# Kernel tuning notes

Hardware: AMD Instinct MI355X
Metric: run time of the kernel (lower is better)

Reference implementation:

```python
import jax, jax.numpy as jnp
import numpy as np

B, L, D, Z, V, N, C = 4, 4096, 1024, 128, 1024, 16, 128
STD = 0.02
LN_EPS = 1e-5


def setup_inputs() -> dict:
    ks = jax.random.split(jax.random.key(0), 12)
    f32 = jnp.float32
    return {
        "x": jax.random.normal(ks[0], (B, L, D), dtype=f32),
        "ln1_g": jnp.ones((D,), f32), "ln1_b": jnp.zeros((D,), f32),
        "delta": jax.random.normal(ks[1], (D, N, 1), dtype=f32),
        "alpha": jax.random.normal(ks[2], (D, N, 1), dtype=f32),
        "beta_e": jax.random.normal(ks[3], (D, N, 1), dtype=f32) * STD,
        "gamma_e": jax.random.normal(ks[4], (D, N), dtype=f32),
        "omega": jax.random.normal(ks[5], (D,), dtype=f32) * STD,
        "Wv": jax.random.normal(ks[6], (D, V), dtype=f32) * STD, "bv": jnp.zeros((V,), f32),
        "Wmx": jax.random.normal(ks[7], (D, Z + V + 2 * D), dtype=f32) * STD, "bmx": jnp.zeros((Z + V + 2 * D,), f32),
        "Wh": jax.random.normal(ks[8], (V, D), dtype=f32) * STD, "bh": jnp.zeros((D,), f32),
        "gamma_g": jax.random.normal(ks[9], (2, Z), dtype=f32) * STD, "beta_g": jnp.zeros((2, Z), f32),
        "rpb": jax.random.normal(ks[10], (2 * C - 1,), dtype=f32) * STD,
        "ln2_g": jnp.ones((D,), f32), "ln2_b": jnp.zeros((D,), f32),
        "W1": jax.random.normal(ks[11], (D, 2 * D), dtype=f32) * STD, "b1": jnp.zeros((2 * D,), f32),
        "W2": jax.random.normal(jax.random.fold_in(ks[11], 1), (2 * D, D), dtype=f32) * STD, "b2": jnp.zeros((D,), f32),
    }


def layer_norm(x, g, b):
    m = jnp.mean(x, axis=-1, keepdims=True)
    xc = x - m
    v = jnp.mean(xc * xc, axis=-1, keepdims=True)
    return xc * jax.lax.rsqrt(v + LN_EPS) * g + b


def multi_head_ema(x, delta, alpha, beta_e, gamma_e, omega):
    # x: (B,L,D). Damped EMA SSM (MEGA), unidirectional, via causal FFT conv.
    p = jax.nn.sigmoid(delta)                      # (D,N,1)
    a = jax.nn.sigmoid(alpha)                      # (D,N,1)
    q = 1.0 - p * a                                # decay in (0,1)
    t = jnp.arange(L, dtype=x.dtype)               # (L,)
    vander = t[None, None, :] * jnp.log(q)         # (D,N,L)
    kern = (p * beta_e) * jnp.exp(vander)          # (D,N,L)
    scale = (1.0 / N) ** 0.5
    k = jnp.einsum('dnl,dn->dl', kern, gamma_e * scale)  # (D,L)
    n_fft = 2 * L
    xf = jnp.fft.rfft(x.transpose(0, 2, 1), n=n_fft)     # (B,D,F)
    kf = jnp.fft.rfft(k, n=n_fft)                        # (D,F)
    out = jnp.fft.irfft(xf * kf[None], n=n_fft)[..., :L] # (B,D,L) causal conv
    return out.transpose(0, 2, 1) + x * omega[None, None, :]


def simple_rel_pos_bias(rpb, c):
    # rpb: (2c-1,) -> (c,c) Toeplitz relative-position bias (MEGA 'simple')
    t = jnp.pad(rpb, (0, c))           # (3c-1,)
    t = jnp.tile(t, c)[:-c]            # (c*(3c-2),)
    t = t.reshape(c, 3 * c - 2)
    r = (2 * c - 1) // 2
    return t[:, r: t.shape[1] - r]     # (c,c)


def reference(x, ln1_g, ln1_b, delta, alpha, beta_e, gamma_e, omega, Wv, bv,
              Wmx, bmx, Wh, bh, gamma_g, beta_g, rpb, ln2_g, ln2_b, W1, b1, W2, b2):
    residual = x
    xn = layer_norm(x, ln1_g, ln1_b)                         # prenorm
    v = jax.nn.silu(xn @ Wv + bv)                            # (B,L,V)
    mx = jax.nn.silu(multi_head_ema(xn, delta, alpha, beta_e, gamma_e, omega))
    base = mx @ Wmx + bmx                                    # (B,L,D+Z+V+D)
    u = jax.nn.sigmoid(base[..., :D])                        # gate
    zr = jax.nn.silu(base[..., D:D + Z + V])
    hx = base[..., D + Z + V:]                               # (B,L,D)
    z, r = zr[..., :Z], zr[..., Z:]                          # (B,L,Z),(B,L,V)
    zz = z[..., None, :] * gamma_g + beta_g                  # (B,L,2,Z)
    q, k = zz[..., 0, :], zz[..., 1, :]
    K = L // C
    qc = q.reshape(B, K, C, Z) * (Z ** -0.5)
    kc = k.reshape(B, K, C, Z)
    vc = v.reshape(B, K, C, V)
    bias = simple_rel_pos_bias(rpb, C)                       # (C,C)
    scores = jnp.einsum('bkcz,bkdz->bkcd', qc, kc) + bias    # (B,K,C,C)
    attn = jax.nn.softmax(scores, axis=-1)
    h = jnp.einsum('bkcd,bkdv->bkcv', attn, vc).reshape(B, L, V)
    h = jax.nn.silu(hx + (h * r) @ Wh + bh)                  # (B,L,D)
    out = residual + u * (h - residual)                      # addcmul gate
    # FFN residual block (prenorm, residual 'R')
    y = layer_norm(out, ln2_g, ln2_b)
    y = jax.nn.silu(y @ W1 + b1) @ W2 + b2
    return out + y
```

## Files before the change

kernel.cpp:

```cpp
#include <hip/hip_runtime.h>
#include <hip/hip_bf16.h>

typedef __attribute__((ext_vector_type(8))) short bf16x8;
typedef __attribute__((ext_vector_type(4))) float f32x4;

#define DEV static __device__ __forceinline__

#define VMW(n) asm volatile("s_waitcnt vmcnt(" #n ")" ::: "memory")
#define BARX   asm volatile("s_barrier" ::: "memory")

DEV float bf2f(unsigned short u) {
    unsigned int x = ((unsigned int)u) << 16;
    return __builtin_bit_cast(float, x);
}
DEV unsigned short f2bf(float f) {
    unsigned int x = __builtin_bit_cast(unsigned int, f);
    unsigned int r = x + 0x7fffu + ((x >> 16) & 1u);
    return (unsigned short)(r >> 16);
}
DEV float sigmoidf_(float x) { return 1.f / (1.f + __expf(-x)); }
DEV float siluf_(float x)    { return x / (1.f + __expf(-x)); }

DEV void llds16(const unsigned short* g, unsigned short* l) {
    __builtin_amdgcn_global_load_lds((const __attribute__((address_space(1))) void*)g,
                                     (__attribute__((address_space(3))) void*)l, 16, 0, 0);
}

DEV void swz_xy(int& bx, int& by) {
    int gx = gridDim.x;
    int ychunk = gridDim.y >> 3;
    int n = blockIdx.y * gx + blockIdx.x;
    int idx = n >> 3;
    bx = idx / ychunk;
    by = (n & 7) * ychunk + (idx % ychunk);
}

DEV void mfma256(const unsigned short* __restrict__ A, const unsigned short* __restrict__ Bt,
                 int lda, int ldb, int KT, unsigned short* lds, f32x4 (&acc)[8][4])
{
    const int tid  = threadIdx.x;
    const int lane = tid & 63;
    const int w    = tid >> 6;
    const int wr   = (w >> 2) << 6;
    const int wc   = (w & 3) << 5;
    const int mr   = lane & 15;
    const int kq   = (lane >> 4) << 4;
    const int srow = tid >> 3;
    const int sw   = ((tid & 7) ^ (srow & 7)) << 3;

    const unsigned short* gA0 = A + (size_t)srow * lda + sw;
    const unsigned short* gA1 = gA0 + (size_t)128 * lda;
    const unsigned short* gB0 = Bt + (size_t)srow * ldb + sw;
    const unsigned short* gB1 = gB0 + (size_t)128 * ldb;
    const size_t a64 = (size_t)64 * lda, b64 = (size_t)64 * ldb;
    unsigned short* dst = lds + tid * 8;

    const int swz = (mr & 7) << 4;
    const int offK0 = kq ^ swz;
    const int offK1 = (64 + kq) ^ swz;
    const char* pAb = (const char*)lds + (wr + mr) * 128;
    const char* pBb = (const char*)lds + 32768 + (wc + mr) * 128;

#define STAGE8(NX) do { \
    unsigned short* d0 = dst + (NX) * 32768; \
    llds16(gA0, d0);          llds16(gA0 + a64, d0 + 4096);  gA0 += 64; \
    llds16(gB0, d0 + 16384);  llds16(gB0 + b64, d0 + 20480); gB0 += 64; \
    llds16(gB1, d0 + 24576);  llds16(gB1 + b64, d0 + 28672); gB1 += 64; \
    llds16(gA1, d0 + 8192);   llds16(gA1 + a64, d0 + 12288); gA1 += 64; \
} while (0)

    STAGE8(0);

    bf16x8 av[4][2], bA[2][2], bB[2][2];
    for (int kt = 0; kt < KT; ++kt) {
        VMW(0);
        BARX;
        if (kt + 1 < KT) STAGE8((kt & 1) ^ 1);
        const char* pA_ = pAb + (kt & 1) * 65536;
        const char* pB_ = pBb + (kt & 1) * 65536;
#pragma unroll
        for (int m = 0; m < 4; ++m) { av[m][0] = *(const bf16x8*)(pA_ + m * 2048 + offK0);
                                      av[m][1] = *(const bf16x8*)(pA_ + m * 2048 + offK1); }
#pragma unroll
        for (int n = 0; n < 2; ++n) { bA[n][0] = *(const bf16x8*)(pB_ + n * 2048 + offK0);
                                      bA[n][1] = *(const bf16x8*)(pB_ + n * 2048 + offK1); }
        __builtin_amdgcn_s_setprio(1);
#pragma unroll
        for (int m = 0; m < 4; ++m)
#pragma unroll
            for (int n = 0; n < 2; ++n) {
                acc[m][n] = __builtin_amdgcn_mfma_f32_16x16x32_bf16(av[m][0], bA[n][0], acc[m][n], 0, 0, 0);
                acc[m][n] = __builtin_amdgcn_mfma_f32_16x16x32_bf16(av[m][1], bA[n][1], acc[m][n], 0, 0, 0);
            }
        __builtin_amdgcn_s_setprio(0);
#pragma unroll
        for (int n = 0; n < 2; ++n) { bB[n][0] = *(const bf16x8*)(pB_ + 16384 + n * 2048 + offK0);
                                      bB[n][1] = *(const bf16x8*)(pB_ + 16384 + n * 2048 + offK1); }
        __builtin_amdgcn_s_setprio(1);
#pragma unroll
        for (int m = 0; m < 4; ++m)
#pragma unroll
            for (int n = 0; n < 2; ++n) {
                acc[m][2 + n] = __builtin_amdgcn_mfma_f32_16x16x32_bf16(av[m][0], bB[n][0], acc[m][2 + n], 0, 0, 0);
                acc[m][2 + n] = __builtin_amdgcn_mfma_f32_16x16x32_bf16(av[m][1], bB[n][1], acc[m][2 + n], 0, 0, 0);
            }
        __builtin_amdgcn_s_setprio(0);
#pragma unroll
        for (int m = 0; m < 4; ++m) { av[m][0] = *(const bf16x8*)(pA_ + 16384 + m * 2048 + offK0);
                                      av[m][1] = *(const bf16x8*)(pA_ + 16384 + m * 2048 + offK1); }
        __builtin_amdgcn_s_setprio(1);
#pragma unroll
        for (int m = 0; m < 4; ++m)
#pragma unroll
            for (int n = 0; n < 2; ++n) {
                acc[4 + m][n] = __builtin_amdgcn_mfma_f32_16x16x32_bf16(av[m][0], bA[n][0], acc[4 + m][n], 0, 0, 0);
                acc[4 + m][n] = __builtin_amdgcn_mfma_f32_16x16x32_bf16(av[m][1], bA[n][1], acc[4 + m][n], 0, 0, 0);
            }
        __builtin_amdgcn_s_setprio(0);
        __builtin_amdgcn_s_setprio(1);
#pragma unroll
        for (int m = 0; m < 4; ++m)
#pragma unroll
            for (int n = 0; n < 2; ++n) {
                acc[4 + m][2 + n] = __builtin_amdgcn_mfma_f32_16x16x32_bf16(av[m][0], bB[n][0], acc[4 + m][2 + n], 0, 0, 0);
                acc[4 + m][2 + n] = __builtin_amdgcn_mfma_f32_16x16x32_bf16(av[m][1], bB[n][1], acc[4 + m][2 + n], 0, 0, 0);
            }
        __builtin_amdgcn_s_setprio(0);
    }
#undef STAGE8
    BARX;
}

template <class F>
DEV void stage_rm(unsigned short* lds, const f32x4 (&acc)[8][4], F f)
{
    const int lane = threadIdx.x & 63, w = threadIdx.x >> 6;
    const int wr = (w >> 2) << 6, wc = (w & 3) << 5;
    const int rsub = (lane >> 4) << 2, csub = lane & 15;
#pragma unroll
    for (int i = 0; i < 8; ++i)
#pragma unroll
        for (int j = 0; j < 4; ++j) {
            int rl = ((i >> 2) << 7) + wr + ((i & 3) << 4) + rsub;
            int cl = ((j >> 1) << 7) + wc + ((j & 1) << 4) + csub;
#pragma unroll
            for (int jj = 0; jj < 4; ++jj) {
                int r = rl + jj;
                *(unsigned short*)((char*)lds + r * 512 + ((cl * 2) ^ (((r >> 2) & 3) << 5))) =
                    f(acc[i][j][jj], cl);
            }
        }
}
template <class F>
DEV void stage_cm(unsigned short* lds, const f32x4 (&acc)[8][4], F f)
{
    const int lane = threadIdx.x & 63, w = threadIdx.x >> 6;
    const int wr = (w >> 2) << 6, wc = (w & 3) << 5;
    const int rsub = (lane >> 4) << 2, csub = lane & 15;
#pragma unroll
    for (int i = 0; i < 8; ++i)
#pragma unroll
        for (int j = 0; j < 4; ++j) {
            int rl = ((i >> 2) << 7) + wr + ((i & 3) << 4) + rsub;
            int cl = ((j >> 1) << 7) + wc + ((j & 1) << 4) + csub;
            ushort4 p;
            p.x = f(acc[i][j][0], cl); p.y = f(acc[i][j][1], cl);
            p.z = f(acc[i][j][2], cl); p.w = f(acc[i][j][3], cl);
            *(ushort4*)((char*)lds + cl * 512 + ((rl * 2) ^ ((cl & 3) << 4))) = p;
        }
}
DEV bf16x8 rd_rm(const unsigned short* lds, int row, int cb) {
    return *(const bf16x8*)((const char*)lds + row * 512 + ((cb * 16) ^ (((row >> 2) & 3) << 5)));
}
DEV bf16x8 rd_cm(const unsigned short* lds, int col, int rb) {
    return *(const bf16x8*)((const char*)lds + col * 512 + ((rb * 16) ^ ((col & 3) << 4)));
}

DEV void mfma_loop(const unsigned short* __restrict__ A, const unsigned short* __restrict__ Bt,
                   int lda, int ldb, int K, unsigned short* lds, f32x4 acc[4][4])
{
    const int tid = threadIdx.x;
    const int lane = tid & 63;
    const int wid = tid >> 6;
    const int wm = wid >> 1, wn = wid & 1;
    const int row0 = tid >> 2,         cg0 = (tid & 3) * 8;
    const int row1 = (256 + tid) >> 2, cg1 = (tid & 3) * 8;
    const int dst0 = (tid - lane) * 8;
    const int dst1 = (256 + tid - lane) * 8;

    auto stage = [&](unsigned short* sbuf, int kt) {
        const unsigned short* gA = A + (size_t)kt * 32;
        const unsigned short* gB = Bt + (size_t)kt * 32;
        llds16(gA + (size_t)row0 * lda + cg0, sbuf + dst0);
        llds16(gA + (size_t)row1 * lda + cg1, sbuf + dst1);
        llds16(gB + (size_t)row0 * ldb + cg0, sbuf + 4096 + dst0);
        llds16(gB + (size_t)row1 * ldb + cg1, sbuf + 4096 + dst1);
    };

    const int KT = K >> 5;
    stage(lds, 0);
    __syncthreads();
    const int mr = lane & 15, kr = (lane >> 4) * 8;
    for (int kt = 0; kt < KT; ++kt) {
        unsigned short* sbuf = lds + (kt & 1) * 8192;
        if (kt + 1 < KT) stage(lds + ((kt + 1) & 1) * 8192, kt + 1);
        const unsigned short* sA = sbuf;
        const unsigned short* sB = sbuf + 4096;
        bf16x8 av[4], bv[4];
#pragma unroll
        for (int f = 0; f < 4; ++f) {
            av[f] = *(const bf16x8*)(sA + (wm * 64 + f * 16 + mr) * 32 + kr);
            bv[f] = *(const bf16x8*)(sB + (wn * 64 + f * 16 + mr) * 32 + kr);
        }
#pragma unroll
        for (int fm = 0; fm < 4; ++fm)
#pragma unroll
            for (int fn = 0; fn < 4; ++fn)
                acc[fm][fn] = __builtin_amdgcn_mfma_f32_16x16x32_bf16(av[fm], bv[fn], acc[fm][fn], 0, 0, 0);
        __syncthreads();
    }
}

__global__ void k_transpose(const float* __restrict__ W, unsigned short* __restrict__ Wt, int K, int N)
{
    __shared__ float tile[32][33];
    int n0 = blockIdx.x * 32, k0 = blockIdx.y * 32;
    for (int i = threadIdx.y; i < 32; i += 8)
        tile[i][threadIdx.x] = W[(size_t)(k0 + i) * N + n0 + threadIdx.x];
    __syncthreads();
    for (int i = threadIdx.y; i < 32; i += 8)
        Wt[(size_t)(n0 + i) * K + k0 + threadIdx.x] = f2bf(tile[threadIdx.x][i]);
}

__global__ __launch_bounds__(256) void k_ln(const float* __restrict__ x, const float* __restrict__ g,
                                            const float* __restrict__ b, unsigned short* __restrict__ o)
{
    size_t row = blockIdx.x;
    int tid = threadIdx.x;
    float4 v = ((const float4*)(x + row * 1024))[tid];
    float s = v.x + v.y + v.z + v.w;
    float sq = v.x * v.x + v.y * v.y + v.z * v.z + v.w * v.w;
#pragma unroll
    for (int off = 1; off < 64; off <<= 1) { s += __shfl_xor(s, off); sq += __shfl_xor(sq, off); }
    __shared__ float ls[4], lq[4];
    int wid = tid >> 6;
    if ((tid & 63) == 0) { ls[wid] = s; lq[wid] = sq; }
    __syncthreads();
    s = ls[0] + ls[1] + ls[2] + ls[3];
    sq = lq[0] + lq[1] + lq[2] + lq[3];
    float mean = s * (1.f / 1024.f);
    float var = sq * (1.f / 1024.f) - mean * mean;
    float rstd = rsqrtf(var + 1e-5f);
    float4 gv = ((const float4*)g)[tid];
    float4 bv = ((const float4*)b)[tid];
    ushort4 p;
    p.x = f2bf((v.x - mean) * rstd * gv.x + bv.x);
    p.y = f2bf((v.y - mean) * rstd * gv.y + bv.y);
    p.z = f2bf((v.z - mean) * rstd * gv.z + bv.z);
    p.w = f2bf((v.w - mean) * rstd * gv.w + bv.w);
    ((ushort4*)(o + row * 1024))[tid] = p;
}

#define SEG 128
#define NSEG 32

__global__ __launch_bounds__(64) void k_ema_a(const unsigned short* __restrict__ xn,
                                              const float* __restrict__ delta, const float* __restrict__ alpha,
                                              float* __restrict__ st)
{
    int d = blockIdx.x * 64 + threadIdx.x;
    int s = blockIdx.y, b = blockIdx.z;
    float q[16], h[16];
#pragma unroll
    for (int n = 0; n < 16; ++n) {
        float p = sigmoidf_(delta[d * 16 + n]);
        float a = sigmoidf_(alpha[d * 16 + n]);
        q[n] = 1.f - p * a; h[n] = 0.f;
    }
    const unsigned short* xp = xn + ((size_t)b * 4096 + (size_t)s * SEG) * 1024 + d;
    for (int l = 0; l < SEG; ++l) {
        float xv = bf2f(xp[(size_t)l * 1024]);
#pragma unroll
        for (int n = 0; n < 16; ++n) h[n] = q[n] * h[n] + xv;
    }
    float* sp = st + (size_t)(b * 1024 + d) * 16 * NSEG;
#pragma unroll
    for (int n = 0; n < 16; ++n) sp[n * NSEG + s] = h[n];
}

__global__ void k_ema_b(const float* __restrict__ delta, const float* __restrict__ alpha, float* __restrict__ st)
{
    int gid = blockIdx.x * 256 + threadIdx.x;
    int n = gid & 15, d = (gid >> 4) & 1023;
    float p = sigmoidf_(delta[d * 16 + n]);
    float a = sigmoidf_(alpha[d * 16 + n]);
    float qq = 1.f - p * a;
    float qs = qq;
#pragma unroll
    for (int i = 0; i < 7; ++i) qs *= qs;
    float* sp = st + (size_t)gid * NSEG;
    float A_ = 0.f;
#pragma unroll
    for (int s = 0; s < NSEG; ++s) { float t = sp[s]; sp[s] = A_; A_ = qs * A_ + t; }
}

__global__ __launch_bounds__(64) void k_ema_c(const unsigned short* __restrict__ xn,
                                              const float* __restrict__ delta, const float* __restrict__ alpha,
                                              const float* __restrict__ beta_e, const float* __restrict__ gamma_e,
                                              const float* __restrict__ omega, const float* __restrict__ st,
                                              unsigned short* __restrict__ mxb)
{
    int d = blockIdx.x * 64 + threadIdx.x;
    int s = blockIdx.y, b = blockIdx.z;
    float q[16], c[16], h[16];
    const float* sp = st + (size_t)(b * 1024 + d) * 16 * NSEG;
#pragma unroll
    for (int n = 0; n < 16; ++n) {
        float p = sigmoidf_(delta[d * 16 + n]);
        float a = sigmoidf_(alpha[d * 16 + n]);
        q[n] = 1.f - p * a;
        c[n] = p * beta_e[d * 16 + n] * gamma_e[d * 16 + n] * 0.25f;
        h[n] = sp[n * NSEG + s];
    }
    float om = omega[d];
    const unsigned short* xp = xn + ((size_t)b * 4096 + (size_t)s * SEG) * 1024 + d;
    unsigned short* op = mxb + ((size_t)b * 4096 + (size_t)s * SEG) * 1024 + d;
    for (int l = 0; l < SEG; ++l) {
        float xv = bf2f(xp[(size_t)l * 1024]);
        float o = xv * om;
#pragma unroll
        for (int n = 0; n < 16; ++n) { h[n] = q[n] * h[n] + xv; o += c[n] * h[n]; }
        op[(size_t)l * 1024] = f2bf(siluf_(o));
    }
}

__global__ __launch_bounds__(512, 2) void k_gemm_v2_v(const unsigned short* __restrict__ xn,
                                                      const unsigned short* __restrict__ WvT,
                                                      const float* __restrict__ bv, unsigned short* __restrict__ vt)
{
    __shared__ __align__(16) unsigned short lds[65536];
    int bx, by; swz_xy(bx, by);
    int n0 = bx * 256, m0 = by * 256;
    f32x4 acc[8][4] = {};
    mfma256(xn + (size_t)m0 * 1024, WvT + (size_t)n0 * 1024, 1024, 1024, 16, lds, acc);
    stage_cm(lds, acc, [&](float v, int cl) -> unsigned short {
        return f2bf(siluf_(v + bv[n0 + cl]));
    });
    __syncthreads();
    const int t = threadIdx.x;
#pragma unroll
    for (int it = 0; it < 16; ++it) {
        int col = it * 16 + (t >> 5);
        int rb = t & 31;
        bf16x8 vv = rd_cm(lds, col, rb);
        int grow = m0 + rb * 8;
        size_t off = ((size_t)(grow >> 7) * 1024 + (n0 + col)) * 128 + (grow & 127);
        *(bf16x8*)(vt + off) = vv;
    }
}

__global__ __launch_bounds__(512, 2) void k_gemm_v2_mx(const unsigned short* __restrict__ mx,
                                                       const unsigned short* __restrict__ WmxT,
                                                       const float* __restrict__ bmx,
                                                       const float* __restrict__ gamma_g, const float* __restrict__ beta_g,
                                                       unsigned short* __restrict__ ub, unsigned short* __restrict__ qb,
                                                       unsigned short* __restrict__ kb, unsigned short* __restrict__ rb,
                                                       unsigned short* __restrict__ hxb)
{
    __shared__ __align__(16) unsigned short lds[65536];
    int bx, by; swz_xy(bx, by);
    int n0 = bx * 256, m0 = by * 256;
    f32x4 acc[8][4] = {};
    mfma256(mx + (size_t)m0 * 1024, WmxT + (size_t)n0 * 1024, 1024, 1024, 16, lds, acc);
    stage_rm(lds, acc, [&](float v, int cl) -> unsigned short {
        int gc = n0 + cl;
        if (gc >= 3200) return 0;
        float val = v + bmx[gc];
        if (gc < 1024) return f2bf(sigmoidf_(val));
        if (gc < 2176) return f2bf(siluf_(val));
        return f2bf(val);
    });
    __syncthreads();
    const int t = threadIdx.x;
#pragma unroll
    for (int it = 0; it < 16; ++it) {
        int row = it * 16 + (t >> 5);
        int cb = t & 31;
        int gc = n0 + cb * 8;
        if (gc >= 3200) continue;
        bf16x8 vv = rd_rm(lds, row, cb);
        size_t grow = m0 + row;
        if (gc < 1024) {
            *(bf16x8*)(ub + grow * 1024 + gc) = vv;
        } else if (gc < 1152) {
            int zc = gc - 1024;
            bf16x8 qv, kv;
#pragma unroll
            for (int e = 0; e < 8; ++e) {
                float z = bf2f((unsigned short)vv[e]);
                qv[e] = (short)f2bf((z * gamma_g[zc + e] + beta_g[zc + e]) * 0.088388347648318447f);
                kv[e] = (short)f2bf(z * gamma_g[128 + zc + e] + beta_g[128 + zc + e]);
            }
            *(bf16x8*)(qb + grow * 128 + zc) = qv;
            *(bf16x8*)(kb + grow * 128 + zc) = kv;
        } else if (gc < 2176) {
            *(bf16x8*)(rb + grow * 1024 + (gc - 1152)) = vv;
        } else {
            *(bf16x8*)(hxb + grow * 1024 + (gc - 2176)) = vv;
        }
    }
}

__global__ __launch_bounds__(256) void k_attn(const unsigned short* __restrict__ qb,
                                              const unsigned short* __restrict__ kb,
                                              const float* __restrict__ rpb, unsigned short* __restrict__ attn)
{
    __shared__ __align__(16) union U { unsigned short stage[16384]; unsigned short sc[128 * 132]; } sh;
    int bc = blockIdx.x;
    size_t t0 = (size_t)bc * 128;
    f32x4 acc[4][4] = {};
    mfma_loop(qb + t0 * 128, kb + t0 * 128, 128, 128, 128, sh.stage, acc);
    int tid = threadIdx.x, lane = tid & 63, wid = tid >> 6, wm = wid >> 1, wn = wid & 1;
#pragma unroll
    for (int fm = 0; fm < 4; ++fm)
#pragma unroll
        for (int fn = 0; fn < 4; ++fn) {
            int r = wm * 64 + fm * 16 + ((lane >> 4) << 2);
            int c = wn * 64 + fn * 16 + (lane & 15);
#pragma unroll
            for (int j = 0; j < 4; ++j) sh.sc[(r + j) * 132 + c] = f2bf(acc[fm][fn][j]);
        }
    __syncthreads();
    int row = tid >> 1, half = tid & 1;
    const unsigned short* srow = sh.sc + row * 132 + half * 64;
    const float* bp = rpb + 127 - row + half * 64;
    float v[64];
    float mxv = -1e30f;
#pragma unroll
    for (int i = 0; i < 64; ++i) { float s = bf2f(srow[i]) + bp[i]; v[i] = s; mxv = fmaxf(mxv, s); }
    mxv = fmaxf(mxv, __shfl_xor(mxv, 1));
    float sum = 0.f;
#pragma unroll
    for (int i = 0; i < 64; ++i) { float e = __expf(v[i] - mxv); v[i] = e; sum += e; }
    sum += __shfl_xor(sum, 1);
    float inv = 1.f / sum;
    unsigned short* arow = attn + ((size_t)bc * 128 + row) * 128 + half * 64;
#pragma unroll
    for (int i = 0; i < 64; ++i) arow[i] = f2bf(v[i] * inv);
}

__global__ __launch_bounds__(256) void k_gemm_pv(const unsigned short* __restrict__ attn,
                                                 const unsigned short* __restrict__ vt,
                                                 unsigned short* __restrict__ rhr)
{
    __shared__ __align__(16) unsigned short lds[16384];
    int bc = blockIdx.z;
    int n0 = blockIdx.x * 128;
    f32x4 acc[4][4] = {};
    mfma_loop(attn + (size_t)bc * 16384, vt + (size_t)bc * 131072 + (size_t)n0 * 128, 128, 128, 128, lds, acc);
    int lane = threadIdx.x & 63, wid = threadIdx.x >> 6, wm = wid >> 1, wn = wid & 1;
#pragma unroll
    for (int fm = 0; fm < 4; ++fm)
#pragma unroll
        for (int fn = 0; fn < 4; ++fn) {
            int rowb = wm * 64 + fm * 16 + ((lane >> 4) << 2);
            int col = n0 + wn * 64 + fn * 16 + (lane & 15);
#pragma unroll
            for (int j = 0; j < 4; ++j) {
                size_t m = (size_t)bc * 128 + rowb + j;
                size_t off = m * 1024 + col;
                rhr[off] = f2bf(acc[fm][fn][j] * bf2f(rhr[off]));
            }
        }
}

__global__ __launch_bounds__(512, 2) void k_gemm_v2_out(const unsigned short* __restrict__ hr,
                                                        const unsigned short* __restrict__ WhT,
                                                        const float* __restrict__ bh,
                                                        const unsigned short* __restrict__ hxb,
                                                        const unsigned short* __restrict__ ub,
                                                        const float* __restrict__ x, float* __restrict__ outp)
{
    __shared__ __align__(16) unsigned short lds[65536];
    int bx, by; swz_xy(bx, by);
    int n0 = bx * 256, m0 = by * 256;
    f32x4 acc[8][4] = {};
    mfma256(hr + (size_t)m0 * 1024, WhT + (size_t)n0 * 1024, 1024, 1024, 16, lds, acc);
    const int lane = threadIdx.x & 63, w = threadIdx.x >> 6;
    const int wr = (w >> 2) << 6, wc = (w & 3) << 5;
    const int rsub = (lane >> 4) << 2, csub = lane & 15;
#pragma unroll
    for (int i = 0; i < 8; ++i)
#pragma unroll
        for (int j = 0; j < 4; ++j) {
            int rowb = m0 + ((i >> 2) << 7) + wr + ((i & 3) << 4) + rsub;
            int col = n0 + ((j >> 1) << 7) + wc + ((j & 1) << 4) + csub;
            float bias = bh[col];
#pragma unroll
            for (int jj = 0; jj < 4; ++jj) {
                size_t off = (size_t)(rowb + jj) * 1024 + col;
                float g = acc[i][j][jj] + bias + bf2f(hxb[off]);
                float h2 = siluf_(g);
                float xv = x[off];
                outp[off] = xv + bf2f(ub[off]) * (h2 - xv);
            }
        }
}

__global__ __launch_bounds__(512, 2) void k_ffn1_v2(const unsigned short* __restrict__ yn,
                                                    const unsigned short* __restrict__ W1T,
                                                    const float* __restrict__ b1, unsigned short* __restrict__ t1)
{
    __shared__ __align__(16) unsigned short lds[65536];
    int bx, by; swz_xy(bx, by);
    int n0 = bx * 256, m0 = by * 256;
    f32x4 acc[8][4] = {};
    mfma256(yn + (size_t)m0 * 1024, W1T + (size_t)n0 * 1024, 1024, 1024, 16, lds, acc);
    stage_rm(lds, acc, [&](float v, int cl) -> unsigned short {
        return f2bf(siluf_(v + b1[n0 + cl]));
    });
    __syncthreads();
    const int t = threadIdx.x;
#pragma unroll
    for (int it = 0; it < 16; ++it) {
        int row = it * 16 + (t >> 5);
        int cb = t & 31;
        bf16x8 vv = rd_rm(lds, row, cb);
        *(bf16x8*)(t1 + (size_t)(m0 + row) * 2048 + n0 + cb * 8) = vv;
    }
}

__global__ __launch_bounds__(512, 2) void k_ffn2_v2(const unsigned short* __restrict__ t1,
                                                    const unsigned short* __restrict__ W2T,
                                                    const float* __restrict__ b2, float* __restrict__ outp)
{
    __shared__ __align__(16) unsigned short lds[65536];
    int bx, by; swz_xy(bx, by);
    int n0 = bx * 256, m0 = by * 256;
    f32x4 acc[8][4] = {};
    mfma256(t1 + (size_t)m0 * 2048, W2T + (size_t)n0 * 2048, 2048, 2048, 32, lds, acc);
    const int lane = threadIdx.x & 63, w = threadIdx.x >> 6;
    const int wr = (w >> 2) << 6, wc = (w & 3) << 5;
    const int rsub = (lane >> 4) << 2, csub = lane & 15;
#pragma unroll
    for (int i = 0; i < 8; ++i)
#pragma unroll
        for (int j = 0; j < 4; ++j) {
            int rowb = m0 + ((i >> 2) << 7) + wr + ((i & 3) << 4) + rsub;
            int col = n0 + ((j >> 1) << 7) + wc + ((j & 1) << 4) + csub;
            float bias = b2[col];
#pragma unroll
            for (int jj = 0; jj < 4; ++jj) {
                size_t off = (size_t)(rowb + jj) * 1024 + col;
                outp[off] = outp[off] + acc[i][j][jj] + bias;
            }
        }
}

extern "C" void kernel_launch(void* const* d_in, const int* in_sizes, int n_in,
                              void* d_out, int out_size, void* d_ws, size_t ws_size,
                              hipStream_t stream)
{
    (void)in_sizes; (void)n_in; (void)out_size; (void)ws_size;
    const float* x      = (const float*)d_in[0];
    const float* ln1_g  = (const float*)d_in[1];
    const float* ln1_b  = (const float*)d_in[2];
    const float* delta  = (const float*)d_in[3];
    const float* alpha  = (const float*)d_in[4];
    const float* beta_e = (const float*)d_in[5];
    const float* gamma_e= (const float*)d_in[6];
    const float* omega  = (const float*)d_in[7];
    const float* Wv     = (const float*)d_in[8];
    const float* bv     = (const float*)d_in[9];
    const float* Wmx    = (const float*)d_in[10];
    const float* bmx    = (const float*)d_in[11];
    const float* Wh     = (const float*)d_in[12];
    const float* bh     = (const float*)d_in[13];
    const float* gamma_g= (const float*)d_in[14];
    const float* beta_g = (const float*)d_in[15];
    const float* rpb    = (const float*)d_in[16];
    const float* ln2_g  = (const float*)d_in[17];
    const float* ln2_b  = (const float*)d_in[18];
    const float* W1     = (const float*)d_in[19];
    const float* b1     = (const float*)d_in[20];
    const float* W2     = (const float*)d_in[21];
    const float* b2     = (const float*)d_in[22];
    float* outp = (float*)d_out;

    char* w = (char*)d_ws;
    unsigned short* xn   = (unsigned short*)(w + 0);
    unsigned short* at   = (unsigned short*)(w + 0);
    unsigned short* mxb  = (unsigned short*)(w + 33554432);
    unsigned short* t1   = (unsigned short*)(w + 0);
    unsigned short* vt   = (unsigned short*)(w + 67108864);
    unsigned short* ub   = (unsigned short*)(w + 100663296);
    unsigned short* hxb  = (unsigned short*)(w + 134217728);
    unsigned short* rb   = (unsigned short*)(w + 167772160);
    unsigned short* yn   = (unsigned short*)(w + 167772160);
    unsigned short* qb   = (unsigned short*)(w + 201326592);
    unsigned short* kb   = (unsigned short*)(w + 205520896);
    float*          st   = (float*)(w + 201326592);
    unsigned short* WvT  = (unsigned short*)(w + 209715200);
    unsigned short* WmxT = (unsigned short*)(w + 211812352);
    unsigned short* WhT  = (unsigned short*)(w + 218628096);
    unsigned short* W1T  = (unsigned short*)(w + 220725248);
    unsigned short* W2T  = (unsigned short*)(w + 224919552);

    dim3 tb(32, 8);
    k_transpose<<<dim3(32, 32), tb, 0, stream>>>(Wv, WvT, 1024, 1024);
    k_transpose<<<dim3(100, 32), tb, 0, stream>>>(Wmx, WmxT, 1024, 3200);
    k_transpose<<<dim3(32, 32), tb, 0, stream>>>(Wh, WhT, 1024, 1024);
    k_transpose<<<dim3(64, 32), tb, 0, stream>>>(W1, W1T, 1024, 2048);
    k_transpose<<<dim3(32, 64), tb, 0, stream>>>(W2, W2T, 2048, 1024);

    k_ln<<<16384, 256, 0, stream>>>(x, ln1_g, ln1_b, xn);

    k_ema_a<<<dim3(16, NSEG, 4), 64, 0, stream>>>(xn, delta, alpha, st);
    k_ema_b<<<256, 256, 0, stream>>>(delta, alpha, st);
    k_ema_c<<<dim3(16, NSEG, 4), 64, 0, stream>>>(xn, delta, alpha, beta_e, gamma_e, omega, st, mxb);

    k_gemm_v2_v<<<dim3(4, 64), 512, 0, stream>>>(xn, WvT, bv, vt);
    k_gemm_v2_mx<<<dim3(13, 64), 512, 0, stream>>>(mxb, WmxT, bmx, gamma_g, beta_g, ub, qb, kb, rb, hxb);
    k_attn<<<128, 256, 0, stream>>>(qb, kb, rpb, at);
    k_gemm_pv<<<dim3(8, 1, 128), 256, 0, stream>>>(at, vt, rb);
    k_gemm_v2_out<<<dim3(4, 64), 512, 0, stream>>>(rb, WhT, bh, hxb, ub, x, outp);
    k_ln<<<16384, 256, 0, stream>>>(outp, ln2_g, ln2_b, yn);
    k_ffn1_v2<<<dim3(8, 64), 512, 0, stream>>>(yn, W1T, b1, t1);
    k_ffn2_v2<<<dim3(4, 64), 512, 0, stream>>>(t1, W2T, b2, outp);
}
```

Before: 646.7 us.

## Use 16-wave 256x256 GEMM blocks with per-wave 64x64 tiles

Replaces the 8-wave 256x256 MFMA mainloop with a 16-wave (1024-thread) version where each wave owns a 64x64 sub-tile, halving accumulator registers per wave. It staggers the K-half order across waves to spread LDS bank traffic, uses __syncthreads instead of manual waitcnt/barrier, and splits the LDS-staged epilogues into two 128-row or 128-column halves because of the new wave layout. The aim is more waves in flight per CU for latency hiding. The trade-off is one block per CU instead of two, and full-block barriers each K step across 16 waves.

After: 1.162 ms. 79.7% more time.

```diff
diff --git a/kernel.cpp b/kernel.cpp
--- a/kernel.cpp
+++ b/kernel.cpp
@@ -5,9 +5,6 @@
 typedef __attribute__((ext_vector_type(4))) float f32x4;
 
 #define DEV static __device__ __forceinline__
-
-#define VMW(n) asm volatile("s_waitcnt vmcnt(" #n ")" ::: "memory")
-#define BARX   asm volatile("s_barrier" ::: "memory")
 
 DEV float bf2f(unsigned short u) {
     unsigned int x = ((unsigned int)u) << 16;
@@ -35,145 +32,72 @@
     by = (n & 7) * ychunk + (idx % ychunk);
 }
 
-DEV void mfma256(const unsigned short* __restrict__ A, const unsigned short* __restrict__ Bt,
-                 int lda, int ldb, int KT, unsigned short* lds, f32x4 (&acc)[8][4])
+DEV void mfma16w(const unsigned short* __restrict__ A, const unsigned short* __restrict__ Bt,
+                 int lda, int ldb, int KT, unsigned short* lds, f32x4 (&acc)[4][4])
 {
     const int tid  = threadIdx.x;
     const int lane = tid & 63;
     const int w    = tid >> 6;
-    const int wr   = (w >> 2) << 6;
-    const int wc   = (w & 3) << 5;
+    const int wm   = w >> 2, wn = w & 3;
     const int mr   = lane & 15;
-    const int kq   = (lane >> 4) << 4;
+    const int kg   = lane >> 4;
+
     const int srow = tid >> 3;
-    const int sw   = ((tid & 7) ^ (srow & 7)) << 3;
-
-    const unsigned short* gA0 = A + (size_t)srow * lda + sw;
+    const int sg   = (tid & 7) ^ (srow & 7);
+    const unsigned short* gA0 = A  + (size_t)srow * lda + sg * 8;
     const unsigned short* gA1 = gA0 + (size_t)128 * lda;
-    const unsigned short* gB0 = Bt + (size_t)srow * ldb + sw;
+    const unsigned short* gB0 = Bt + (size_t)srow * ldb + sg * 8;
     const unsigned short* gB1 = gB0 + (size_t)128 * ldb;
-    const size_t a64 = (size_t)64 * lda, b64 = (size_t)64 * ldb;
-    unsigned short* dst = lds + tid * 8;
-
-    const int swz = (mr & 7) << 4;
-    const int offK0 = kq ^ swz;
-    const int offK1 = (64 + kq) ^ swz;
-    const char* pAb = (const char*)lds + (wr + mr) * 128;
-    const char* pBb = (const char*)lds + 32768 + (wc + mr) * 128;
-
-#define STAGE8(NX) do { \
-    unsigned short* d0 = dst + (NX) * 32768; \
-    llds16(gA0, d0);          llds16(gA0 + a64, d0 + 4096);  gA0 += 64; \
-    llds16(gB0, d0 + 16384);  llds16(gB0 + b64, d0 + 20480); gB0 += 64; \
-    llds16(gB1, d0 + 24576);  llds16(gB1 + b64, d0 + 28672); gB1 += 64; \
-    llds16(gA1, d0 + 8192);   llds16(gA1 + a64, d0 + 12288); gA1 += 64; \
-} while (0)
-
-    STAGE8(0);
-
-    bf16x8 av[4][2], bA[2][2], bB[2][2];
+    unsigned short* dA0 = lds + tid * 8;
+    unsigned short* dA1 = dA0 + 8192;
+    unsigned short* dB0 = dA0 + 16384;
+    unsigned short* dB1 = dA0 + 24576;
+
+    const int swz  = (mr & 7) << 4;
+    const int off0 = (kg << 4) ^ swz;
+    const int off1 = (64 + (kg << 4)) ^ swz;
+    const char* pAr = (const char*)lds + (wm * 64 + mr) * 128;
+    const char* pBr = (const char*)lds + 32768 + (wn * 64 + mr) * 128;
+    const int stag = (w ^ (w >> 2)) & 1;
+
+    auto stage = [&](int nb) {
+        int o = nb * 32768;
+        llds16(gA0, dA0 + o); gA0 += 64;
+        llds16(gA1, dA1 + o); gA1 += 64;
+        llds16(gB0, dB0 + o); gB0 += 64;
+        llds16(gB1, dB1 + o); gB1 += 64;
+    };
+
+    bf16x8 av[4], bv[4];
+    auto halfK = [&](const char* pa, const char* pb, int off) {
+#pragma unroll
+        for (int f = 0; f < 4; ++f) {
+            av[f] = *(const bf16x8*)(pa + f * 2048 + off);
+            bv[f] = *(const bf16x8*)(pb + f * 2048 + off);
+        }
+        __builtin_amdgcn_s_setprio(1);
+#pragma unroll
+        for (int fm = 0; fm < 4; ++fm)
+#pragma unroll
+            for (int fn = 0; fn < 4; ++fn)
+                acc[fm][fn] = __builtin_amdgcn_mfma_f32_16x16x32_bf16(av[fm], bv[fn], acc[fm][fn], 0, 0, 0);
+        __builtin_amdgcn_s_setprio(0);
+    };
+
+    stage(0);
+    __syncthreads();
     for (int kt = 0; kt < KT; ++kt) {
-        VMW(0);
-        BARX;
-        if (kt + 1 < KT) STAGE8((kt & 1) ^ 1);
-        const char* pA_ = pAb + (kt & 1) * 65536;
-        const char* pB_ = pBb + (kt & 1) * 65536;
-#pragma unroll
-        for (int m = 0; m < 4; ++m) { av[m][0] = *(const bf16x8*)(pA_ + m * 2048 + offK0);
-                                      av[m][1] = *(const bf16x8*)(pA_ + m * 2048 + offK1); }
-#pragma unroll
-        for (int n = 0; n < 2; ++n) { bA[n][0] = *(const bf16x8*)(pB_ + n * 2048 + offK0);
-                                      bA[n][1] = *(const bf16x8*)(pB_ + n * 2048 + offK1); }
-        __builtin_amdgcn_s_setprio(1);
-#pragma unroll
-        for (int m = 0; m < 4; ++m)
-#pragma unroll
-            for (int n = 0; n < 2; ++n) {
-                acc[m][n] = __builtin_amdgcn_mfma_f32_16x16x32_bf16(av[m][0], bA[n][0], acc[m][n], 0, 0, 0);
-                acc[m][n] = __builtin_amdgcn_mfma_f32_16x16x32_bf16(av[m][1], bA[n][1], acc[m][n], 0, 0, 0);
-            }
-        __builtin_amdgcn_s_setprio(0);
-#pragma unroll
-        for (int n = 0; n < 2; ++n) { bB[n][0] = *(const bf16x8*)(pB_ + 16384 + n * 2048 + offK0);
-                                      bB[n][1] = *(const bf16x8*)(pB_ + 16384 + n * 2048 + offK1); }
-        __builtin_amdgcn_s_setprio(1);
-#pragma unroll
-        for (int m = 0; m < 4; ++m)
-#pragma unroll
-            for (int n = 0; n < 2; ++n) {
-                acc[m][2 + n] = __builtin_amdgcn_mfma_f32_16x16x32_bf16(av[m][0], bB[n][0], acc[m][2 + n], 0, 0, 0);
-                acc[m][2 + n] = __builtin_amdgcn_mfma_f32_16x16x32_bf16(av[m][1], bB[n][1], acc[m][2 + n], 0, 0, 0);
-            }
-        __builtin_amdgcn_s_setprio(0);
-#pragma unroll
-        for (int m = 0; m < 4; ++m) { av[m][0] = *(const bf16x8*)(pA_ + 16384 + m * 2048 + offK0);
-                                      av[m][1] = *(const bf16x8*)(pA_ + 16384 + m * 2048 + offK1); }
-        __builtin_amdgcn_s_setprio(1);
-#pragma unroll
-        for (int m = 0; m < 4; ++m)
-#pragma unroll
-            for (int n = 0; n < 2; ++n) {
-                acc[4 + m][n] = __builtin_amdgcn_mfma_f32_16x16x32_bf16(av[m][0], bA[n][0], acc[4 + m][n], 0, 0, 0);
-                acc[4 + m][n] = __builtin_amdgcn_mfma_f32_16x16x32_bf16(av[m][1], bA[n][1], acc[4 + m][n], 0, 0, 0);
-            }
-        __builtin_amdgcn_s_setprio(0);
-        __builtin_amdgcn_s_setprio(1);
-#pragma unroll
-        for (int m = 0; m < 4; ++m)
-#pragma unroll
-            for (int n = 0; n < 2; ++n) {
-                acc[4 + m][2 + n] = __builtin_amdgcn_mfma_f32_16x16x32_bf16(av[m][0], bB[n][0], acc[4 + m][2 + n], 0, 0, 0);
-                acc[4 + m][2 + n] = __builtin_amdgcn_mfma_f32_16x16x32_bf16(av[m][1], bB[n][1], acc[4 + m][2 + n], 0, 0, 0);
-            }
-        __builtin_amdgcn_s_setprio(0);
-    }
-#undef STAGE8
-    BARX;
-}
-
-template <class F>
-DEV void stage_rm(unsigned short* lds, const f32x4 (&acc)[8][4], F f)
-{
-    const int lane = threadIdx.x & 63, w = threadIdx.x >> 6;
-    const int wr = (w >> 2) << 6, wc = (w & 3) << 5;
-    const int rsub = (lane >> 4) << 2, csub = lane & 15;
-#pragma unroll
-    for (int i = 0; i < 8; ++i)
-#pragma unroll
-        for (int j = 0; j < 4; ++j) {
-            int rl = ((i >> 2) << 7) + wr + ((i & 3) << 4) + rsub;
-            int cl = ((j >> 1) << 7) + wc + ((j & 1) << 4) + csub;
-#pragma unroll
-            for (int jj = 0; jj < 4; ++jj) {
-                int r = rl + jj;
-                *(unsigned short*)((char*)lds + r * 512 + ((cl * 2) ^ (((r >> 2) & 3) << 5))) =
-                    f(acc[i][j][jj], cl);
-            }
-        }
-}
-template <class F>
-DEV void stage_cm(unsigned short* lds, const f32x4 (&acc)[8][4], F f)
-{
-    const int lane = threadIdx.x & 63, w = threadIdx.x >> 6;
-    const int wr = (w >> 2) << 6, wc = (w & 3) << 5;
-    const int rsub = (lane >> 4) << 2, csub = lane & 15;
-#pragma unroll
-    for (int i = 0; i < 8; ++i)
-#pragma unroll
-        for (int j = 0; j < 4; ++j) {
-            int rl = ((i >> 2) << 7) + wr + ((i & 3) << 4) + rsub;
-            int cl = ((j >> 1) << 7) + wc + ((j & 1) << 4) + csub;
-            ushort4 p;
-            p.x = f(acc[i][j][0], cl); p.y = f(acc[i][j][1], cl);
-            p.z = f(acc[i][j][2], cl); p.w = f(acc[i][j][3], cl);
-            *(ushort4*)((char*)lds + cl * 512 + ((rl * 2) ^ ((cl & 3) << 4))) = p;
-        }
-}
+        if (kt + 1 < KT) stage((kt + 1) & 1);
+        const char* pa = pAr + (kt & 1) * 65536;
+        const char* pb = pBr + (kt & 1) * 65536;
+        if (stag) { halfK(pa, pb, off1); halfK(pa, pb, off0); }
+        else      { halfK(pa, pb, off0); halfK(pa, pb, off1); }
+        __syncthreads();
+    }
+}
+
 DEV bf16x8 rd_rm(const unsigned short* lds, int row, int cb) {
     return *(const bf16x8*)((const char*)lds + row * 512 + ((cb * 16) ^ (((row >> 2) & 3) << 5)));
-}
-DEV bf16x8 rd_cm(const unsigned short* lds, int col, int rb) {
-    return *(const bf16x8*)((const char*)lds + col * 512 + ((rb * 16) ^ ((col & 3) << 4)));
 }
 
 DEV void mfma_loop(const unsigned short* __restrict__ A, const unsigned short* __restrict__ Bt,
@@ -252,12 +176,12 @@
     float var = sq * (1.f / 1024.f) - mean * mean;
     float rstd = rsqrtf(var + 1e-5f);
     float4 gv = ((const float4*)g)[tid];
-    float4 bv = ((const float4*)b)[tid];
+    float4 bvv = ((const float4*)b)[tid];
     ushort4 p;
-    p.x = f2bf((v.x - mean) * rstd * gv.x + bv.x);
-    p.y = f2bf((v.y - mean) * rstd * gv.y + bv.y);
-    p.z = f2bf((v.z - mean) * rstd * gv.z + bv.z);
-    p.w = f2bf((v.w - mean) * rstd * gv.w + bv.w);
+    p.x = f2bf((v.x - mean) * rstd * gv.x + bvv.x);
+    p.y = f2bf((v.y - mean) * rstd * gv.y + bvv.y);
+    p.z = f2bf((v.z - mean) * rstd * gv.z + bvv.z);
+    p.w = f2bf((v.w - mean) * rstd * gv.w + bvv.w);
     ((ushort4*)(o + row * 1024))[tid] = p;
 }
 
@@ -334,80 +258,120 @@
     }
 }
 
-__global__ __launch_bounds__(512, 2) void k_gemm_v2_v(const unsigned short* __restrict__ xn,
-                                                      const unsigned short* __restrict__ WvT,
-                                                      const float* __restrict__ bv, unsigned short* __restrict__ vt)
+__global__ __launch_bounds__(1024) void k_gemm_v2_v(const unsigned short* __restrict__ xn,
+                                                    const unsigned short* __restrict__ WvT,
+                                                    const float* __restrict__ bv, unsigned short* __restrict__ vt)
 {
     __shared__ __align__(16) unsigned short lds[65536];
     int bx, by; swz_xy(bx, by);
     int n0 = bx * 256, m0 = by * 256;
-    f32x4 acc[8][4] = {};
-    mfma256(xn + (size_t)m0 * 1024, WvT + (size_t)n0 * 1024, 1024, 1024, 16, lds, acc);
-    stage_cm(lds, acc, [&](float v, int cl) -> unsigned short {
-        return f2bf(siluf_(v + bv[n0 + cl]));
-    });
-    __syncthreads();
-    const int t = threadIdx.x;
-#pragma unroll
-    for (int it = 0; it < 16; ++it) {
-        int col = it * 16 + (t >> 5);
-        int rb = t & 31;
-        bf16x8 vv = rd_cm(lds, col, rb);
-        int grow = m0 + rb * 8;
-        size_t off = ((size_t)(grow >> 7) * 1024 + (n0 + col)) * 128 + (grow & 127);
-        *(bf16x8*)(vt + off) = vv;
-    }
-}
-
-__global__ __launch_bounds__(512, 2) void k_gemm_v2_mx(const unsigned short* __restrict__ mx,
-                                                       const unsigned short* __restrict__ WmxT,
-                                                       const float* __restrict__ bmx,
-                                                       const float* __restrict__ gamma_g, const float* __restrict__ beta_g,
-                                                       unsigned short* __restrict__ ub, unsigned short* __restrict__ qb,
-                                                       unsigned short* __restrict__ kb, unsigned short* __restrict__ rb,
-                                                       unsigned short* __restrict__ hxb)
+    f32x4 acc[4][4] = {};
+    mfma16w(xn + (size_t)m0 * 1024, WvT + (size_t)n0 * 1024, 1024, 1024, 16, lds, acc);
+    const int t = threadIdx.x, lane = t & 63, w = t >> 6;
+    const int wm = w >> 2, wn = w & 3;
+    const int rsub = (lane >> 4) << 2, csub = lane & 15;
+    for (int h = 0; h < 2; ++h) {
+        if ((wn >> 1) == h) {
+            int cl0 = (wn & 1) * 64;
+#pragma unroll
+            for (int fm = 0; fm < 4; ++fm)
+#pragma unroll
+                for (int fn = 0; fn < 4; ++fn) {
+                    int rl = wm * 64 + fm * 16 + rsub;
+                    int cl = cl0 + fn * 16 + csub;
+                    float bias = bv[n0 + h * 128 + cl];
+                    ushort4 p;
+                    p.x = f2bf(siluf_(acc[fm][fn][0] + bias));
+                    p.y = f2bf(siluf_(acc[fm][fn][1] + bias));
+                    p.z = f2bf(siluf_(acc[fm][fn][2] + bias));
+                    p.w = f2bf(siluf_(acc[fm][fn][3] + bias));
+                    *(ushort4*)((char*)lds + cl * 512 + ((rl * 2) ^ ((cl & 3) << 4))) = p;
+                }
+        }
+        __syncthreads();
+#pragma unroll
+        for (int it = 0; it < 4; ++it) {
+            int col = it * 32 + (t >> 5);
+            int rb = t & 31;
+            bf16x8 vv = *(const bf16x8*)((const char*)lds + col * 512 + ((rb * 16) ^ ((col & 3) << 4)));
+            int grow = m0 + rb * 8;
+            size_t off = ((size_t)(grow >> 7) * 1024 + (n0 + h * 128 + col)) * 128 + (grow & 127);
+            *(bf16x8*)(vt + off) = vv;
+        }
+        __syncthreads();
+    }
+}
+
+__global__ __launch_bounds__(1024) void k_gemm_v2_mx(const unsigned short* __restrict__ mx,
+                                                     const unsigned short* __restrict__ WmxT,
+                                                     const float* __restrict__ bmx,
+                                                     const float* __restrict__ gamma_g, const float* __restrict__ beta_g,
+                                                     unsigned short* __restrict__ ub, unsigned short* __restrict__ qb,
+                                                     unsigned short* __restrict__ kb, unsigned short* __restrict__ rb,
+                                                     unsigned short* __restrict__ hxb)
 {
     __shared__ __align__(16) unsigned short lds[65536];
     int bx, by; swz_xy(bx, by);
     int n0 = bx * 256, m0 = by * 256;
-    f32x4 acc[8][4] = {};
-    mfma256(mx + (size_t)m0 * 1024, WmxT + (size_t)n0 * 1024, 1024, 1024, 16, lds, acc);
-    stage_rm(lds, acc, [&](float v, int cl) -> unsigned short {
-        int gc = n0 + cl;
-        if (gc >= 3200) return 0;
-        float val = v + bmx[gc];
-        if (gc < 1024) return f2bf(sigmoidf_(val));
-        if (gc < 2176) return f2bf(siluf_(val));
-        return f2bf(val);
-    });
-    __syncthreads();
-    const int t = threadIdx.x;
-#pragma unroll
-    for (int it = 0; it < 16; ++it) {
-        int row = it * 16 + (t >> 5);
-        int cb = t & 31;
-        int gc = n0 + cb * 8;
-        if (gc >= 3200) continue;
-        bf16x8 vv = rd_rm(lds, row, cb);
-        size_t grow = m0 + row;
-        if (gc < 1024) {
-            *(bf16x8*)(ub + grow * 1024 + gc) = vv;
-        } else if (gc < 1152) {
-            int zc = gc - 1024;
-            bf16x8 qv, kv;
-#pragma unroll
-            for (int e = 0; e < 8; ++e) {
-                float z = bf2f((unsigned short)vv[e]);
-                qv[e] = (short)f2bf((z * gamma_g[zc + e] + beta_g[zc + e]) * 0.088388347648318447f);
-                kv[e] = (short)f2bf(z * gamma_g[128 + zc + e] + beta_g[128 + zc + e]);
+    f32x4 acc[4][4] = {};
+    mfma16w(mx + (size_t)m0 * 1024, WmxT + (size_t)n0 * 1024, 1024, 1024, 16, lds, acc);
+    const int t = threadIdx.x, lane = t & 63, w = t >> 6;
+    const int wm = w >> 2, wn = w & 3;
+    const int rsub = (lane >> 4) << 2, csub = lane & 15;
+    for (int h = 0; h < 2; ++h) {
+        if ((wm >> 1) == h) {
+            int rl0 = (wm & 1) * 64;
+#pragma unroll
+            for (int fm = 0; fm < 4; ++fm)
+#pragma unroll
+                for (int fn = 0; fn < 4; ++fn) {
+                    int rl = rl0 + fm * 16 + rsub;
+                    int cl = wn * 64 + fn * 16 + csub;
+                    int gc = n0 + cl;
+                    float bias = (gc < 3200) ? bmx[gc] : 0.f;
+#pragma unroll
+                    for (int jj = 0; jj < 4; ++jj) {
+                        int r = rl + jj;
+                        float val = acc[fm][fn][jj] + bias;
+                        unsigned short o;
+                        if (gc >= 3200)      o = 0;
+                        else if (gc < 1024)  o = f2bf(sigmoidf_(val));
+                        else if (gc < 2176)  o = f2bf(siluf_(val));
+                        else                 o = f2bf(val);
+                        *(unsigned short*)((char*)lds + r * 512 + ((cl * 2) ^ (((r >> 2) & 3) << 5))) = o;
+                    }
+                }
+        }
+        __syncthreads();
+#pragma unroll
+        for (int it = 0; it < 4; ++it) {
+            int row = it * 32 + (t >> 5);
+            int cb = t & 31;
+            int gc = n0 + cb * 8;
+            if (gc < 3200) {
+                bf16x8 vv = rd_rm(lds, row, cb);
+                size_t grow = m0 + h * 128 + row;
+                if (gc < 1024) {
+                    *(bf16x8*)(ub + grow * 1024 + gc) = vv;
+                } else if (gc < 1152) {
+                    int zc = gc - 1024;
+                    bf16x8 qv, kv;
+#pragma unroll
+                    for (int e = 0; e < 8; ++e) {
+                        float z = bf2f((unsigned short)vv[e]);
+                        qv[e] = (short)f2bf((z * gamma_g[zc + e] + beta_g[zc + e]) * 0.088388347648318447f);
+                        kv[e] = (short)f2bf(z * gamma_g[128 + zc + e] + beta_g[128 + zc + e]);
+                    }
+                    *(bf16x8*)(qb + grow * 128 + zc) = qv;
+                    *(bf16x8*)(kb + grow * 128 + zc) = kv;
+                } else if (gc < 2176) {
+                    *(bf16x8*)(rb + grow * 1024 + (gc - 1152)) = vv;
+                } else {
+                    *(bf16x8*)(hxb + grow * 1024 + (gc - 2176)) = vv;
+                }
             }
-            *(bf16x8*)(qb + grow * 128 + zc) = qv;
-            *(bf16x8*)(kb + grow * 128 + zc) = kv;
-        } else if (gc < 2176) {
-            *(bf16x8*)(rb + grow * 1024 + (gc - 1152)) = vv;
-        } else {
-            *(bf16x8*)(hxb + grow * 1024 + (gc - 2176)) = vv;
-        }
+        }
+        __syncthreads();
     }
 }
 
@@ -474,32 +438,32 @@
         }
 }
 
-__global__ __launch_bounds__(512, 2) void k_gemm_v2_out(const unsigned short* __restrict__ hr,
-                                                        const unsigned short* __restrict__ WhT,
-                                                        const float* __restrict__ bh,
-                                                        const unsigned short* __restrict__ hxb,
-                                                        const unsigned short* __restrict__ ub,
-                                                        const float* __restrict__ x, float* __restrict__ outp)
+__global__ __launch_bounds__(1024) void k_gemm_v2_out(const unsigned short* __restrict__ hr,
+                                                      const unsigned short* __restrict__ WhT,
+                                                      const float* __restrict__ bh,
+                                                      const unsigned short* __restrict__ hxb,
+                                                      const unsigned short* __restrict__ ub,
+                                                      const float* __restrict__ x, float* __restrict__ outp)
 {
     __shared__ __align__(16) unsigned short lds[65536];
     int bx, by; swz_xy(bx, by);
     int n0 = bx * 256, m0 = by * 256;
-    f32x4 acc[8][4] = {};
-    mfma256(hr + (size_t)m0 * 1024, WhT + (size_t)n0 * 1024, 1024, 1024, 16, lds, acc);
+    f32x4 acc[4][4] = {};
+    mfma16w(hr + (size_t)m0 * 1024, WhT + (size_t)n0 * 1024, 1024, 1024, 16, lds, acc);
     const int lane = threadIdx.x & 63, w = threadIdx.x >> 6;
-    const int wr = (w >> 2) << 6, wc = (w & 3) << 5;
+    const int wm = w >> 2, wn = w & 3;
     const int rsub = (lane >> 4) << 2, csub = lane & 15;
 #pragma unroll
-    for (int i = 0; i < 8; ++i)
-#pragma unroll
-        for (int j = 0; j < 4; ++j) {
-            int rowb = m0 + ((i >> 2) << 7) + wr + ((i & 3) << 4) + rsub;
-            int col = n0 + ((j >> 1) << 7) + wc + ((j & 1) << 4) + csub;
+    for (int fm = 0; fm < 4; ++fm)
+#pragma unroll
+        for (int fn = 0; fn < 4; ++fn) {
+            int rowb = m0 + wm * 64 + fm * 16 + rsub;
+            int col = n0 + wn * 64 + fn * 16 + csub;
             float bias = bh[col];
 #pragma unroll
             for (int jj = 0; jj < 4; ++jj) {
                 size_t off = (size_t)(rowb + jj) * 1024 + col;
-                float g = acc[i][j][jj] + bias + bf2f(hxb[off]);
+                float g = acc[fm][fn][jj] + bias + bf2f(hxb[off]);
                 float h2 = siluf_(g);
                 float xv = x[off];
                 outp[off] = xv + bf2f(ub[off]) * (h2 - xv);
@@ -507,52 +471,71 @@
         }
 }
 
-__global__ __launch_bounds__(512, 2) void k_ffn1_v2(const unsigned short* __restrict__ yn,
-                                                    const unsigned short* __restrict__ W1T,
-                                                    const float* __restrict__ b1, unsigned short* __restrict__ t1)
+__global__ __launch_bounds__(1024) void k_ffn1_v2(const unsigned short* __restrict__ yn,
+                                                  const unsigned short* __restrict__ W1T,
+                                                  const float* __restrict__ b1, unsigned short* __restrict__ t1)
 {
     __shared__ __align__(16) unsigned short lds[65536];
     int bx, by; swz_xy(bx, by);
     int n0 = bx * 256, m0 = by * 256;
-    f32x4 acc[8][4] = {};
-    mfma256(yn + (size_t)m0 * 1024, W1T + (size_t)n0 * 1024, 1024, 1024, 16, lds, acc);
-    stage_rm(lds, acc, [&](float v, int cl) -> unsigned short {
-        return f2bf(siluf_(v + b1[n0 + cl]));
-    });
-    __syncthreads();
-    const int t = threadIdx.x;
-#pragma unroll
-    for (int it = 0; it < 16; ++it) {
-        int row = it * 16 + (t >> 5);
-        int cb = t & 31;
-        bf16x8 vv = rd_rm(lds, row, cb);
-        *(bf16x8*)(t1 + (size_t)(m0 + row) * 2048 + n0 + cb * 8) = vv;
-    }
-}
-
-__global__ __launch_bounds__(512, 2) void k_ffn2_v2(const unsigned short* __restrict__ t1,
-                                                    const unsigned short* __restrict__ W2T,
-                                                    const float* __restrict__ b2, float* __restrict__ outp)
+    f32x4 acc[4][4] = {};
+    mfma16w(yn + (size_t)m0 * 1024, W1T + (size_t)n0 * 1024, 1024, 1024, 16, lds, acc);
+    const int t = threadIdx.x, lane = t & 63, w = t >> 6;
+    const int wm = w >> 2, wn = w & 3;
+    const int rsub = (lane >> 4) << 2, csub = lane & 15;
+    for (int h = 0; h < 2; ++h) {
+        if ((wm >> 1) == h) {
+            int rl0 = (wm & 1) * 64;
+#pragma unroll
+            for (int fm = 0; fm < 4; ++fm)
+#pragma unroll
+                for (int fn = 0; fn < 4; ++fn) {
+                    int rl = rl0 + fm * 16 + rsub;
+                    int cl = wn * 64 + fn * 16 + csub;
+                    float bias = b1[n0 + cl];
+#pragma unroll
+                    for (int jj = 0; jj < 4; ++jj) {
+                        int r = rl + jj;
+                        *(unsigned short*)((char*)lds + r * 512 + ((cl * 2) ^ (((r >> 2) & 3) << 5))) =
+                            f2bf(siluf_(acc[fm][fn][jj] + bias));
+                    }
+                }
+        }
+        __syncthreads();
+#pragma unroll
+        for (int it = 0; it < 4; ++it) {
+            int row = it * 32 + (t >> 5);
+            int cb = t & 31;
+            bf16x8 vv = rd_rm(lds, row, cb);
+            *(bf16x8*)(t1 + (size_t)(m0 + h * 128 + row) * 2048 + n0 + cb * 8) = vv;
+        }
+        __syncthreads();
+    }
+}
+
+__global__ __launch_bounds__(1024) void k_ffn2_v2(const unsigned short* __restrict__ t1,
+                                                  const unsigned short* __restrict__ W2T,
+                                                  const float* __restrict__ b2, float* __restrict__ outp)
 {
     __shared__ __align__(16) unsigned short lds[65536];
     int bx, by; swz_xy(bx, by);
     int n0 = bx * 256, m0 = by * 256;
-    f32x4 acc[8][4] = {};
-    mfma256(t1 + (size_t)m0 * 2048, W2T + (size_t)n0 * 2048, 2048, 2048, 32, lds, acc);
+    f32x4 acc[4][4] = {};
+    mfma16w(t1 + (size_t)m0 * 2048, W2T + (size_t)n0 * 2048, 2048, 2048, 32, lds, acc);
     const int lane = threadIdx.x & 63, w = threadIdx.x >> 6;
-    const int wr = (w >> 2) << 6, wc = (w & 3) << 5;
+    const int wm = w >> 2, wn = w & 3;
     const int rsub = (lane >> 4) << 2, csub = lane & 15;
 #pragma unroll
-    for (int i = 0; i < 8; ++i)
-#pragma unroll
-        for (int j = 0; j < 4; ++j) {
-            int rowb = m0 + ((i >> 2) << 7) + wr + ((i & 3) << 4) + rsub;
-            int col = n0 + ((j >> 1) << 7) + wc + ((j & 1) << 4) + csub;
+    for (int fm = 0; fm < 4; ++fm)
+#pragma unroll
+        for (int fn = 0; fn < 4; ++fn) {
+            int rowb = m0 + wm * 64 + fm * 16 + rsub;
+            int col = n0 + wn * 64 + fn * 16 + csub;
             float bias = b2[col];
 #pragma unroll
             for (int jj = 0; jj < 4; ++jj) {
                 size_t off = (size_t)(rowb + jj) * 1024 + col;
-                outp[off] = outp[off] + acc[i][j][jj] + bias;
+                outp[off] = outp[off] + acc[fm][fn][jj] + bias;
             }
         }
 }
@@ -619,12 +602,12 @@
     k_ema_b<<<256, 256, 0, stream>>>(delta, alpha, st);
     k_ema_c<<<dim3(16, NSEG, 4), 64, 0, stream>>>(xn, delta, alpha, beta_e, gamma_e, omega, st, mxb);
 
-    k_gemm_v2_v<<<dim3(4, 64), 512, 0, stream>>>(xn, WvT, bv, vt);
-    k_gemm_v2_mx<<<dim3(13, 64), 512, 0, stream>>>(mxb, WmxT, bmx, gamma_g, beta_g, ub, qb, kb, rb, hxb);
+    k_gemm_v2_v<<<dim3(4, 64), 1024, 0, stream>>>(xn, WvT, bv, vt);
+    k_gemm_v2_mx<<<dim3(13, 64), 1024, 0, stream>>>(mxb, WmxT, bmx, gamma_g, beta_g, ub, qb, kb, rb, hxb);
     k_attn<<<128, 256, 0, stream>>>(qb, kb, rpb, at);
     k_gemm_pv<<<dim3(8, 1, 128), 256, 0, stream>>>(at, vt, rb);
-    k_gemm_v2_out<<<dim3(4, 64), 512, 0, stream>>>(rb, WhT, bh, hxb, ub, x, outp);
+    k_gemm_v2_out<<<dim3(4, 64), 1024, 0, stream>>>(rb, WhT, bh, hxb, ub, x, outp);
     k_ln<<<16384, 256, 0, stream>>>(outp, ln2_g, ln2_b, yn);
-    k_ffn1_v2<<<dim3(8, 64), 512, 0, stream>>>(yn, W1T, b1, t1);
-    k_ffn2_v2<<<dim3(4, 64), 512, 0, stream>>>(t1, W2T, b2, outp);
-}
+    k_ffn1_v2<<<dim3(8, 64), 1024, 0, stream>>>(yn, W1T, b1, t1);
+    k_ffn2_v2<<<dim3(4, 64), 1024, 0, stream>>>(t1, W2T, b2, outp);
+}
```
